# Kernel optimization log

Hardware: AMD Instinct MI355X
Metric: run time of the kernel (lower is better)

Reference implementation:

```python
import jax, jax.numpy as jnp
import numpy as np

B, N, E, D, AD = 2, 4096, 4, 64, 32


def setup_inputs() -> dict:
    key = jax.random.key(0)
    ks = jax.random.split(key, 10)
    s = 0.02  # init std matching module _initialization
    return {
        "prop_state": jax.random.normal(ks[0], (B, N, D), jnp.float32),
        "annotation": jax.random.normal(ks[1], (B, N, AD), jnp.float32),
        "A": jax.random.uniform(ks[2], (B, N, N * E), jnp.float32),
        "W_in": jax.random.normal(ks[3], (E, D, D), jnp.float32) * s,
        "b_in": jnp.zeros((E, D), jnp.float32),
        "Wr": jax.random.normal(ks[4], (D, 2 * D), jnp.float32) * s,
        "br": jnp.zeros((D,), jnp.float32),
        "Wz": jax.random.normal(ks[5], (D, 2 * D), jnp.float32) * s,
        "bz": jnp.zeros((D,), jnp.float32),
        "Wh": jax.random.normal(ks[6], (D, 2 * D), jnp.float32) * s,
        "bh": jnp.zeros((D,), jnp.float32),
        "Wo1": jax.random.normal(ks[7], (D, D + AD), jnp.float32) * s,
        "bo1": jnp.zeros((D,), jnp.float32),
        "Wo2": jax.random.normal(ks[8], (1, D), jnp.float32) * s,
        "bo2": jnp.zeros((1,), jnp.float32),
    }


def reference(prop_state, annotation, A, W_in, b_in, Wr, br, Wz, bz, Wh, bh, Wo1, bo1, Wo2, bo2):
    b, n, d = prop_state.shape
    e = W_in.shape[0]
    # per-edge-type input transforms: [B, E, N, D] -> [B, E*N, D] (edge-type major)
    in_states = jnp.einsum('bnd,eod->beno', prop_state, W_in) + b_in[None, :, None, :]
    in_flat = in_states.reshape(b, e * n, d)
    # dense adjacency aggregation: A [B, N, N*E] x in_flat [B, N*E, D]
    a_in = jnp.einsum('bnm,bmd->bnd', A, in_flat)
    # GRU-style gated node update
    a = jnp.concatenate([a_in, prop_state], axis=-1)  # [B, N, 2D]
    r = jax.nn.sigmoid(a @ Wr.T + br)
    z = jax.nn.sigmoid(a @ Wz.T + bz)
    h_hat = jnp.tanh(jnp.concatenate([a_in, r * prop_state], axis=-1) @ Wh.T + bh)
    new_state = (1.0 - z) * prop_state + z * h_hat  # [B, N, D]
    # output head
    join = jnp.concatenate([new_state, annotation], axis=-1)  # [B, N, D+AD]
    h = jnp.tanh(join @ Wo1.T + bo1)
    out = (h @ Wo2.T + bo2).sum(axis=2)  # [B, N]
    return out
```

## Files before the change

### kernel.cpp

```cpp
#include <hip/hip_runtime.h>
#include <hip/hip_bf16.h>
#include <stdint.h>

typedef __bf16 bf16x8 __attribute__((ext_vector_type(8)));
typedef float  f32x16 __attribute__((ext_vector_type(16)));
typedef float  f32x4  __attribute__((ext_vector_type(4)));

static constexpr int Bz = 2, Nn = 4096, Ee = 4, Dd = 64, ADim = 32;
static constexpr int Mm = Nn * Ee;
static constexpr int KSEG = 4;
static constexpr int KLEN = Mm / KSEG;
static constexpr int NT = Bz * Nn / 32;
static constexpr size_t SEGSTRIDE = (size_t)NT * 32 * 64;
static constexpr int PHK = 256;
static constexpr int NPH = KLEN / PHK;

__device__ __forceinline__ bf16x8 cvt8(float4 a, float4 b) {
  bf16x8 r;
  r[0] = (__bf16)a.x; r[1] = (__bf16)a.y; r[2] = (__bf16)a.z; r[3] = (__bf16)a.w;
  r[4] = (__bf16)b.x; r[5] = (__bf16)b.y; r[6] = (__bf16)b.z; r[7] = (__bf16)b.w;
  return r;
}
__device__ __forceinline__ bf16x8 cvt8v(f32x4 a, f32x4 b) {
  bf16x8 r;
  r[0] = (__bf16)a[0]; r[1] = (__bf16)a[1]; r[2] = (__bf16)a[2]; r[3] = (__bf16)a[3];
  r[4] = (__bf16)b[0]; r[5] = (__bf16)b[1]; r[6] = (__bf16)b[2]; r[7] = (__bf16)b[3];
  return r;
}
__device__ __forceinline__ f32x16 zero16() {
  f32x16 z;
#pragma unroll
  for (int i = 0; i < 16; ++i) z[i] = 0.f;
  return z;
}
__device__ __forceinline__ f32x16 mm(bf16x8 a, bf16x8 b, f32x16 c) {
  return __builtin_amdgcn_mfma_f32_32x32x16_bf16(a, b, c, 0, 0, 0);
}
__device__ __forceinline__ float sigm(float x) { return 1.f / (1.f + __expf(-x)); }
__device__ __forceinline__ float tanh_fast(float x) {
  float e = __expf(2.f * x);
  return 1.f - 2.f / (e + 1.f);
}
__device__ __forceinline__ void async_lds16(const void* g, void* l) {
  __builtin_amdgcn_global_load_lds(
      (const __attribute__((address_space(1))) uint32_t*)g,
      (__attribute__((address_space(3))) uint32_t*)l, 16, 0, 0);
}

__global__ __launch_bounds__(64) void k_pack(
    const float* __restrict__ Wr, const float* __restrict__ Wz,
    const float* __restrict__ Wh, const float* __restrict__ Wo1,
    __bf16* __restrict__ Wp) {
  const int f = blockIdx.x, l = threadIdx.x;
  const int r31 = l & 31, h = l >> 5;
  const float* W; int L, fl;
  if (f < 16)      { W = Wr;  L = 128; fl = f; }
  else if (f < 32) { W = Wz;  L = 128; fl = f - 16; }
  else if (f < 48) { W = Wh;  L = 128; fl = f - 32; }
  else             { W = Wo1; L = 96;  fl = f - 48; }
  const int ks = fl >> 1, oh = fl & 1;
  const float* src = W + (size_t)(32 * oh + r31) * L + 16 * ks + 8 * h;
  float4 s0 = *reinterpret_cast<const float4*>(src);
  float4 s1 = *reinterpret_cast<const float4*>(src + 4);
  *reinterpret_cast<bf16x8*>(Wp + ((size_t)f * 64 + l) * 8) = cvt8(s0, s1);
}

__global__ __launch_bounds__(256) void k_build_bt(
    const float* __restrict__ prop, const float* __restrict__ Win,
    const float* __restrict__ bin, __bf16* __restrict__ Bt) {
  const int nchunk = blockIdx.x;
  const int e = blockIdx.y, b = blockIdx.z;
  const int tid = threadIdx.x;
  const int w = tid >> 6, l = tid & 63;
  const int r31 = l & 31, h = l >> 5;
  const int oh = w & 1, ns = w >> 1;
  const int o_row = oh * 32 + r31;
  const int n_col = nchunk * 64 + ns * 32 + r31;
  const float* wbase = Win + ((size_t)e * 64 + o_row) * 64 + 8 * h;
  const float* pbase = prop + ((size_t)b * Nn + n_col) * 64 + 8 * h;
  f32x16 acc = zero16();
#pragma unroll
  for (int ks = 0; ks < 4; ++ks) {
    float4 w0 = *reinterpret_cast<const float4*>(wbase + 16 * ks);
    float4 w1 = *reinterpret_cast<const float4*>(wbase + 16 * ks + 4);
    float4 p0 = *reinterpret_cast<const float4*>(pbase + 16 * ks);
    float4 p1 = *reinterpret_cast<const float4*>(pbase + 16 * ks + 4);
    acc = mm(cvt8(w0, w1), cvt8(p0, p1), acc);
  }
#pragma unroll
  for (int reg = 0; reg < 16; ++reg) {
    int orow = oh * 32 + (reg & 3) + 8 * (reg >> 2) + 4 * h;
    float v = acc[reg] + bin[e * 64 + orow];
    Bt[((size_t)b * 64 + orow) * Mm + (size_t)e * Nn + n_col] = (__bf16)v;
  }
}

__global__ __launch_bounds__(512, 1) void k_big_gemm(
    const float* __restrict__ A, const __bf16* __restrict__ Bt,
    float* __restrict__ part) {
  __shared__ float  at[4][32][PHK];
  __shared__ __bf16 btl[64][PHK];

  const int bid = blockIdx.x;
  const int kseg = bid & 3;
  const int bb   = (bid >> 2) & 1;
  const int g    = bid >> 3;
  const int ph0  = g & 15;
  const int tid = threadIdx.x;
  const int w = tid >> 6, l = tid & 63;
  const int r31 = l & 31, h = l >> 5;
  const int t = w >> 1, q = w & 1;
  const int n0 = (g * 4 + t) * 32;
  const int tile = bb * 128 + g * 4 + t;
  const size_t kbase = (size_t)kseg * KLEN;

  const float*  Abase = A + ((size_t)(bb * Nn + n0)) * Mm + kbase;
  const __bf16* BtB   = Bt + (size_t)bb * 64 * Mm + kbase;

#define ISSUE_A(p)                                                         \
  { _Pragma("unroll")                                                      \
    for (int j_ = 0; j_ < 16; ++j_) {                                      \
      const int row_ = 16 * q + j_;                                        \
      const float* src_ = Abase + (size_t)row_ * Mm + (size_t)(p) * PHK +  \
                          ((l ^ (row_ & 7)) * 4);                          \
      async_lds16(src_, (void*)&at[t][row_][0]);                           \
    } }
#define ISSUE_BT(p)                                                        \
  { _Pragma("unroll")                                                      \
    for (int i_ = 0; i_ < 4; ++i_) {                                       \
      const int rbase_ = 2 * (4 * w + i_);                                 \
      const int row_ = rbase_ + (l >> 5);                                  \
      const __bf16* src_ = BtB + (size_t)row_ * Mm + (size_t)(p) * PHK +   \
                           (((l & 31) ^ (row_ & 7)) * 8);                  \
      async_lds16(src_, (void*)&btl[rbase_][0]);                           \
    } }

  f32x16 acc = zero16();
  ISSUE_A(ph0);
  ISSUE_BT(ph0);

  const int swz = r31 & 7;
  const int brow = 32 * q + r31;

  for (int pp = 0; pp < NPH; ++pp) {
    asm volatile("s_waitcnt vmcnt(0)" ::: "memory");
    __syncthreads();
#pragma unroll
    for (int s = 0; s < 16; ++s) {
      const int u0 = 4 * s + 2 * h;
      f32x4 fa0 = *reinterpret_cast<const f32x4*>(&at[t][r31][(u0 ^ swz) * 4]);
      f32x4 fa1 = *reinterpret_cast<const f32x4*>(&at[t][r31][((u0 + 1) ^ swz) * 4]);
      bf16x8 fb = *reinterpret_cast<const bf16x8*>(&btl[brow][((2 * s + h) ^ swz) * 8]);
      acc = mm(cvt8v(fa0, fa1), fb, acc);
    }
    __syncthreads();
    if (pp + 1 < NPH) {
      const int pn = (pp + 1 + ph0) & 15;
      ISSUE_A(pn);
      ISSUE_BT(pn);
    }
  }
#undef ISSUE_A
#undef ISSUE_BT

  float* pb = part + (size_t)kseg * SEGSTRIDE + (size_t)tile * 32 * 64 + 32 * q;
#pragma unroll
  for (int reg = 0; reg < 16; ++reg) {
    int row = (reg & 3) + 8 * (reg >> 2) + 4 * h;
    pb[row * 64 + r31] = acc[reg];
  }
}

__global__ __launch_bounds__(64) void k_gru(
    const float* __restrict__ part, const float* __restrict__ prop,
    const float* __restrict__ annot, const __bf16* __restrict__ Wp,
    const float* __restrict__ br, const float* __restrict__ bz,
    const float* __restrict__ bh, const float* __restrict__ bo1,
    const float* __restrict__ Wo2, const float* __restrict__ bo2,
    float* __restrict__ out) {
  __shared__ float plds[32][68];
  __shared__ float tlds[32][68];
  const int tile = blockIdx.x;
  const int R0 = tile * 32;
  const int l = threadIdx.x;
  const int r31 = l & 31, h = l >> 5;

  bf16x8 xa[4], xp[4], xan[2];
  {
    const float* pt = part + ((size_t)tile * 32 + r31) * 64 + 8 * h;
    const float* pb = prop + (size_t)(R0 + r31) * 64 + 8 * h;
#pragma unroll
    for (int ks = 0; ks < 4; ++ks) {
      f32x4 s0, s1;
      s0[0] = s0[1] = s0[2] = s0[3] = 0.f;
      s1[0] = s1[1] = s1[2] = s1[3] = 0.f;
#pragma unroll
      for (int seg = 0; seg < KSEG; ++seg) {
        const float* pp = pt + seg * SEGSTRIDE + 16 * ks;
        f32x4 v0 = *reinterpret_cast<const f32x4*>(pp);
        f32x4 v1 = *reinterpret_cast<const f32x4*>(pp + 4);
        s0[0] += v0[0]; s0[1] += v0[1]; s0[2] += v0[2]; s0[3] += v0[3];
        s1[0] += v1[0]; s1[1] += v1[1]; s1[2] += v1[2]; s1[3] += v1[3];
      }
      xa[ks] = cvt8v(s0, s1);
      float4 p0 = *reinterpret_cast<const float4*>(pb + 16 * ks);
      float4 p1 = *reinterpret_cast<const float4*>(pb + 16 * ks + 4);
      xp[ks] = cvt8(p0, p1);
      *reinterpret_cast<float4*>(&plds[r31][16 * ks + 8 * h]) = p0;
      *reinterpret_cast<float4*>(&plds[r31][16 * ks + 8 * h + 4]) = p1;
    }
    const float* anb = annot + (size_t)(R0 + r31) * ADim + 8 * h;
#pragma unroll
    for (int ks = 0; ks < 2; ++ks) {
      float4 a0 = *reinterpret_cast<const float4*>(anb + 16 * ks);
      float4 a1 = *reinterpret_cast<const float4*>(anb + 16 * ks + 4);
      xan[ks] = cvt8(a0, a1);
    }
  }
  __syncthreads();

#define LDWP(base, ks, oh) \
  (*reinterpret_cast<const bf16x8*>(Wp + (((size_t)(base) + (ks) * 2 + (oh)) * 64 + l) * 8))

  f32x16 aR[2] = {zero16(), zero16()}, aZ[2] = {zero16(), zero16()};
#pragma unroll
  for (int ks = 0; ks < 8; ++ks) {
    bf16x8 af = (ks < 4) ? xa[ks] : xp[ks - 4];
#pragma unroll
    for (int oh = 0; oh < 2; ++oh) {
      aR[oh] = mm(af, LDWP(0, ks, oh), aR[oh]);
      aZ[oh] = mm(af, LDWP(16, ks, oh), aZ[oh]);
    }
  }
  const float br_[2] = {br[r31], br[32 + r31]};
  const float bz_[2] = {bz[r31], bz[32 + r31]};
  float propv[2][16], zv[2][16];
#pragma unroll
  for (int oh = 0; oh < 2; ++oh) {
#pragma unroll
    for (int reg = 0; reg < 16; ++reg) {
      int row = (reg & 3) + 8 * (reg >> 2) + 4 * h;
      int o = 32 * oh + r31;
      propv[oh][reg] = plds[row][o];
      float rv = sigm(aR[oh][reg] + br_[oh]);
      zv[oh][reg] = sigm(aZ[oh][reg] + bz_[oh]);
      tlds[row][o] = rv * propv[oh][reg];
    }
  }
  __syncthreads();
  bf16x8 xr[4];
#pragma unroll
  for (int ks = 0; ks < 4; ++ks) {
    float4 t0 = *reinterpret_cast<const float4*>(&tlds[r31][16 * ks + 8 * h]);
    float4 t1 = *reinterpret_cast<const float4*>(&tlds[r31][16 * ks + 8 * h + 4]);
    xr[ks] = cvt8(t0, t1);
  }
  f32x16 aH[2] = {zero16(), zero16()};
#pragma unroll
  for (int ks = 0; ks < 8; ++ks) {
    bf16x8 af = (ks < 4) ? xa[ks] : xr[ks - 4];
#pragma unroll
    for (int oh = 0; oh < 2; ++oh) aH[oh] = mm(af, LDWP(32, ks, oh), aH[oh]);
  }
  __syncthreads();
  const float bh_[2] = {bh[r31], bh[32 + r31]};
#pragma unroll
  for (int oh = 0; oh < 2; ++oh) {
#pragma unroll
    for (int reg = 0; reg < 16; ++reg) {
      int row = (reg & 3) + 8 * (reg >> 2) + 4 * h;
      int o = 32 * oh + r31;
      float hh = tanh_fast(aH[oh][reg] + bh_[oh]);
      float z = zv[oh][reg];
      tlds[row][o] = (1.f - z) * propv[oh][reg] + z * hh;
    }
  }
  __syncthreads();
  bf16x8 xn[4];
#pragma unroll
  for (int ks = 0; ks < 4; ++ks) {
    float4 t0 = *reinterpret_cast<const float4*>(&tlds[r31][16 * ks + 8 * h]);
    float4 t1 = *reinterpret_cast<const float4*>(&tlds[r31][16 * ks + 8 * h + 4]);
    xn[ks] = cvt8(t0, t1);
  }
  f32x16 aO[2] = {zero16(), zero16()};
#pragma unroll
  for (int ks = 0; ks < 6; ++ks) {
    bf16x8 af = (ks < 4) ? xn[ks] : xan[ks - 4];
#pragma unroll
    for (int oh = 0; oh < 2; ++oh) aO[oh] = mm(af, LDWP(48, ks, oh), aO[oh]);
  }
  const float bo1_[2] = {bo1[r31], bo1[32 + r31]};
  const float wo2_[2] = {Wo2[r31], Wo2[32 + r31]};
  const float bo2v = bo2[0];
#pragma unroll
  for (int reg = 0; reg < 16; ++reg) {
    float h0 = tanh_fast(aO[0][reg] + bo1_[0]);
    float h1 = tanh_fast(aO[1][reg] + bo1_[1]);
    float p = h0 * wo2_[0] + h1 * wo2_[1];
#pragma unroll
    for (int mks = 16; mks >= 1; mks >>= 1) p += __shfl_xor(p, mks, 64);
    if (r31 == 0) {
      int row = (reg & 3) + 8 * (reg >> 2) + 4 * h;
      out[R0 + row] = p + bo2v;
    }
  }
#undef LDWP
}

extern "C" void kernel_launch(void* const* d_in, const int* in_sizes, int n_in,
                              void* d_out, int out_size, void* d_ws, size_t ws_size,
                              hipStream_t stream) {
  const float* prop  = (const float*)d_in[0];
  const float* annot = (const float*)d_in[1];
  const float* A     = (const float*)d_in[2];
  const float* Win   = (const float*)d_in[3];
  const float* bin   = (const float*)d_in[4];
  const float* Wr    = (const float*)d_in[5];
  const float* br    = (const float*)d_in[6];
  const float* Wz    = (const float*)d_in[7];
  const float* bz    = (const float*)d_in[8];
  const float* Wh    = (const float*)d_in[9];
  const float* bh    = (const float*)d_in[10];
  const float* Wo1   = (const float*)d_in[11];
  const float* bo1   = (const float*)d_in[12];
  const float* Wo2   = (const float*)d_in[13];
  const float* bo2   = (const float*)d_in[14];
  float* out = (float*)d_out;

  char* ws = (char*)d_ws;
  __bf16* Bt   = (__bf16*)ws;
  float*  part = (float*)(ws + (size_t)4 * 1024 * 1024);
  __bf16* Wp   = (__bf16*)(ws + (size_t)12 * 1024 * 1024);

  k_pack<<<dim3(60), 64, 0, stream>>>(Wr, Wz, Wh, Wo1, Wp);
  k_build_bt<<<dim3(Nn / 64, Ee, Bz), 256, 0, stream>>>(prop, Win, bin, Bt);
  k_big_gemm<<<dim3(256), 512, 0, stream>>>(A, Bt, part);
  k_gru<<<dim3(NT), 64, 0, stream>>>(part, prop, annot, Wp,
                                     br, bz, bh, bo1, Wo2, bo2, out);
}
```

Measured before the change: 138.3 us.

## Double-buffer A tiles, load Bt fragments from global, split K across waves

The big GEMM kernel now uses two K segments instead of four. Each block covers two 32-row tiles and double-buffers the fp32 A tiles in LDS, so the next phase's async loads overlap the current MFMAs through a partial vmcnt wait. The bf16 Bt fragments are read straight from global memory into registers instead of being staged in LDS. Waves split each phase's K range in half and combine their partial sums through LDS at the end. This is meant to hide A-load latency and reduce the partial-sum traffic, at the cost of redundant global Bt reads and more register pressure.

```diff
diff --git a/kernel.cpp b/kernel.cpp
--- a/kernel.cpp
+++ b/kernel.cpp
@@ -8,7 +8,7 @@
 
 static constexpr int Bz = 2, Nn = 4096, Ee = 4, Dd = 64, ADim = 32;
 static constexpr int Mm = Nn * Ee;
-static constexpr int KSEG = 4;
+static constexpr int KSEG = 2;
 static constexpr int KLEN = Mm / KSEG;
 static constexpr int NT = Bz * Nn / 32;
 static constexpr size_t SEGSTRIDE = (size_t)NT * 32 * 64;
@@ -98,76 +98,91 @@
 __global__ __launch_bounds__(512, 1) void k_big_gemm(
     const float* __restrict__ A, const __bf16* __restrict__ Bt,
     float* __restrict__ part) {
-  __shared__ float  at[4][32][PHK];
-  __shared__ __bf16 btl[64][PHK];
+  __shared__ float at[2][2][32][PHK];
 
   const int bid = blockIdx.x;
-  const int kseg = bid & 3;
-  const int bb   = (bid >> 2) & 1;
-  const int g    = bid >> 3;
-  const int ph0  = g & 15;
+  const int kseg = bid & 1;
+  const int bb   = (bid >> 1) & 1;
+  const int g    = bid >> 2;
+  const int ph0  = g & (NPH - 1);
   const int tid = threadIdx.x;
   const int w = tid >> 6, l = tid & 63;
   const int r31 = l & 31, h = l >> 5;
-  const int t = w >> 1, q = w & 1;
-  const int n0 = (g * 4 + t) * 32;
-  const int tile = bb * 128 + g * 4 + t;
+  const int t = w >> 2, q = (w >> 1) & 1, kh = w & 1;
   const size_t kbase = (size_t)kseg * KLEN;
-
-  const float*  Abase = A + ((size_t)(bb * Nn + n0)) * Mm + kbase;
+  const int tile = bb * 128 + g * 2 + t;
+
+  const float*  Abase = A + (size_t)bb * Nn * Mm + kbase;
   const __bf16* BtB   = Bt + (size_t)bb * 64 * Mm + kbase;
 
-#define ISSUE_A(p)                                                         \
-  { _Pragma("unroll")                                                      \
-    for (int j_ = 0; j_ < 16; ++j_) {                                      \
-      const int row_ = 16 * q + j_;                                        \
-      const float* src_ = Abase + (size_t)row_ * Mm + (size_t)(p) * PHK +  \
-                          ((l ^ (row_ & 7)) * 4);                          \
-      async_lds16(src_, (void*)&at[t][row_][0]);                           \
+#define ISSUE_A(p, buf)                                                     \
+  { _Pragma("unroll")                                                       \
+    for (int j_ = 0; j_ < 8; ++j_) {                                        \
+      const int rw_ = 8 * w + j_;                                           \
+      const int t_ = rw_ >> 5, r_ = rw_ & 31;                               \
+      const float* src_ = Abase +                                           \
+          (size_t)((g * 2 + t_) * 32 + r_) * Mm + (size_t)(p) * PHK +       \
+          ((l ^ (r_ & 7)) * 4);                                             \
+      async_lds16(src_, (void*)&at[buf][t_][r_][0]);                        \
     } }
-#define ISSUE_BT(p)                                                        \
-  { _Pragma("unroll")                                                      \
-    for (int i_ = 0; i_ < 4; ++i_) {                                       \
-      const int rbase_ = 2 * (4 * w + i_);                                 \
-      const int row_ = rbase_ + (l >> 5);                                  \
-      const __bf16* src_ = BtB + (size_t)row_ * Mm + (size_t)(p) * PHK +   \
-                           (((l & 31) ^ (row_ & 7)) * 8);                  \
-      async_lds16(src_, (void*)&btl[rbase_][0]);                           \
-    } }
 
   f32x16 acc = zero16();
-  ISSUE_A(ph0);
-  ISSUE_BT(ph0);
+  ISSUE_A(ph0, 0);
 
   const int swz = r31 & 7;
-  const int brow = 32 * q + r31;
+  const int ubase = kh * 32;
+  const __bf16* fbbase = BtB + (size_t)(32 * q + r31) * Mm + kh * 128 + 8 * h;
 
   for (int pp = 0; pp < NPH; ++pp) {
-    asm volatile("s_waitcnt vmcnt(0)" ::: "memory");
+    const int pr = (pp + ph0) & (NPH - 1);
+    const int bufc = pp & 1;
+    bf16x8 fb[8];
+    const __bf16* fbp = fbbase + (size_t)pr * PHK;
+#pragma unroll
+    for (int s = 0; s < 8; ++s)
+      fb[s] = *reinterpret_cast<const bf16x8*>(fbp + 16 * s);
+    if (pp + 1 < NPH) {
+      const int pn = (pp + 1 + ph0) & (NPH - 1);
+      ISSUE_A(pn, bufc ^ 1);
+      asm volatile("s_waitcnt vmcnt(8)" ::: "memory");
+    } else {
+      asm volatile("s_waitcnt vmcnt(0)" ::: "memory");
+    }
     __syncthreads();
 #pragma unroll
-    for (int s = 0; s < 16; ++s) {
-      const int u0 = 4 * s + 2 * h;
-      f32x4 fa0 = *reinterpret_cast<const f32x4*>(&at[t][r31][(u0 ^ swz) * 4]);
-      f32x4 fa1 = *reinterpret_cast<const f32x4*>(&at[t][r31][((u0 + 1) ^ swz) * 4]);
-      bf16x8 fb = *reinterpret_cast<const bf16x8*>(&btl[brow][((2 * s + h) ^ swz) * 8]);
-      acc = mm(cvt8v(fa0, fa1), fb, acc);
+    for (int s = 0; s < 8; ++s) {
+      const int u0 = ubase + 4 * s + 2 * h;
+      f32x4 fa0 = *reinterpret_cast<const f32x4*>(&at[bufc][t][r31][(u0 ^ swz) * 4]);
+      f32x4 fa1 = *reinterpret_cast<const f32x4*>(&at[bufc][t][r31][((u0 + 1) ^ swz) * 4]);
+      acc = mm(cvt8v(fa0, fa1), fb[s], acc);
     }
     __syncthreads();
-    if (pp + 1 < NPH) {
-      const int pn = (pp + 1 + ph0) & 15;
-      ISSUE_A(pn);
-      ISSUE_BT(pn);
-    }
   }
 #undef ISSUE_A
-#undef ISSUE_BT
-
-  float* pb = part + (size_t)kseg * SEGSTRIDE + (size_t)tile * 32 * 64 + 32 * q;
-#pragma unroll
-  for (int reg = 0; reg < 16; ++reg) {
-    int row = (reg & 3) + 8 * (reg >> 2) + 4 * h;
-    pb[row * 64 + r31] = acc[reg];
+
+  float* red = &at[0][0][0][0];
+  float* rs = red + (t * 2 + q) * 1024 + l * 16;
+  if (kh == 1) {
+#pragma unroll
+    for (int i = 0; i < 4; ++i) {
+      f32x4 v; v[0] = acc[4 * i]; v[1] = acc[4 * i + 1];
+      v[2] = acc[4 * i + 2]; v[3] = acc[4 * i + 3];
+      *reinterpret_cast<f32x4*>(rs + 4 * i) = v;
+    }
+  }
+  __syncthreads();
+  if (kh == 0) {
+    float* pb = part + (size_t)kseg * SEGSTRIDE + (size_t)tile * 32 * 64 + 32 * q;
+#pragma unroll
+    for (int i = 0; i < 4; ++i) {
+      f32x4 v = *reinterpret_cast<const f32x4*>(rs + 4 * i);
+#pragma unroll
+      for (int jj = 0; jj < 4; ++jj) {
+        int reg = 4 * i + jj;
+        int row = (reg & 3) + 8 * (reg >> 2) + 4 * h;
+        pb[row * 64 + r31] = acc[reg] + v[jj];
+      }
+    }
   }
 }
 
```

Result: slower. 161.4 us (+16.7%).
